# Performance work log

Hardware: AMD Instinct MI355X
Metric: run time of the kernel (lower is better)

The kernel has to match this reference:

```python
import jax, jax.numpy as jnp
import numpy as np

EPS = 1e-5
NPOINT = 1024
NSAMPLE = 32


def _bn(x, gamma, beta, axes):
    # batch-norm in training mode (biased variance), channel-last
    m = jnp.mean(x, axes, keepdims=True)
    v = jnp.var(x, axes, keepdims=True)
    return (x - m) * jax.lax.rsqrt(v + EPS) * gamma + beta


def _fps(xyz, npoint):
    # xyz: [B, N, 3] -> indices [B, npoint]; deterministic start at index 0
    xyz = jax.lax.stop_gradient(xyz)
    B, N, _ = xyz.shape

    def step(carry, _):
        dist, far = carry
        c = jnp.take_along_axis(xyz, far[:, None, None], axis=1)  # [B,1,3]
        d = jnp.sum((xyz - c) ** 2, -1)                            # [B,N]
        dist = jnp.minimum(dist, d)
        return (dist, jnp.argmax(dist, -1).astype(jnp.int32)), far

    init = (jnp.full((B, N), 1e10, xyz.dtype), jnp.zeros((B,), jnp.int32))
    _, idx = jax.lax.scan(step, init, None, length=npoint)
    return idx.T  # [B, npoint]


def _sqdist(src, dst):
    # [B,S,C],[B,N,C] -> [B,S,N]
    d = -2.0 * jnp.einsum('bsc,bnc->bsn', src, dst)
    d += jnp.sum(src ** 2, -1)[:, :, None]
    d += jnp.sum(dst ** 2, -1)[:, None, :]
    return d


def _gather(p, idx):
    # p: [B,N,C], idx: [B,...] -> [B,...,C]
    return jax.vmap(lambda a, i: a[i])(p, idx)


def setup_inputs() -> dict:
    key = jax.random.key(0)
    ks = jax.random.split(key, 12)
    B, N, D = 8, 4096, 64
    inp = {
        'xyz': jax.random.normal(ks[0], (B, 3, N), jnp.float32),
        'points': jax.random.normal(ks[1], (B, D, N), jnp.float32),
        # mlp convs (1x1 Conv2d == per-point linear): [out,in]
        'c1_w': jax.random.normal(ks[2], (64, 64), jnp.float32) / 8.0,
        'c1_b': jnp.zeros((64,), jnp.float32),
        'g1': jnp.ones((64,), jnp.float32), 'b1': jnp.zeros((64,), jnp.float32),
        'c2_w': jax.random.normal(ks[3], (128, 64), jnp.float32) / 8.0,
        'c2_b': jnp.zeros((128,), jnp.float32),
        'g2': jnp.ones((128,), jnp.float32), 'b2': jnp.zeros((128,), jnp.float32),
        # weightnet: 3 -> 8 -> 8 -> 16
        'w0_w': jax.random.normal(ks[4], (8, 3), jnp.float32) / np.sqrt(3.0),
        'w0_b': jnp.zeros((8,), jnp.float32),
        'w0_g': jnp.ones((8,), jnp.float32), 'w0_be': jnp.zeros((8,), jnp.float32),
        'w1_w': jax.random.normal(ks[5], (8, 8), jnp.float32) / np.sqrt(8.0),
        'w1_b': jnp.zeros((8,), jnp.float32),
        'w1_g': jnp.ones((8,), jnp.float32), 'w1_be': jnp.zeros((8,), jnp.float32),
        'w2_w': jax.random.normal(ks[6], (16, 8), jnp.float32) / np.sqrt(8.0),
        'w2_b': jnp.zeros((16,), jnp.float32),
        'w2_g': jnp.ones((16,), jnp.float32), 'w2_be': jnp.zeros((16,), jnp.float32),
        # final linear: 16*128 -> 128
        'lin_w': jax.random.normal(ks[7], (128, 16 * 128), jnp.float32) / np.sqrt(2048.0),
        'lin_b': jnp.zeros((128,), jnp.float32),
        'lg': jnp.ones((128,), jnp.float32), 'lb': jnp.zeros((128,), jnp.float32),
    }
    return inp


def reference(xyz, points, c1_w, c1_b, g1, b1, c2_w, c2_b, g2, b2,
              w0_w, w0_b, w0_g, w0_be, w1_w, w1_b, w1_g, w1_be,
              w2_w, w2_b, w2_g, w2_be, lin_w, lin_b, lg, lb):
    B = xyz.shape[0]
    X = jnp.transpose(xyz, (0, 2, 1))      # [B,N,3]
    P = jnp.transpose(points, (0, 2, 1))   # [B,N,D]

    fps_idx = _fps(X, NPOINT)                                      # [B,S]
    new_xyz = jnp.take_along_axis(X, fps_idx[:, :, None], axis=1)  # [B,S,3]

    sqr = _sqdist(jax.lax.stop_gradient(new_xyz), jax.lax.stop_gradient(X))
    _, nidx = jax.lax.top_k(-sqr, NSAMPLE)                         # [B,S,K]

    neigh_xyz = _gather(X, nidx)                                   # [B,S,K,3]
    off = neigh_xyz - new_xyz[:, :, None, :]                       # [B,S,K,3]
    f = _gather(P, nidx)                                           # [B,S,K,D]

    # per-point MLP (1x1 convs + BN2d over (B,K,S) + relu)
    for W, bias, g, be in ((c1_w, c1_b, g1, b1), (c2_w, c2_b, g2, b2)):
        f = jax.nn.relu(_bn(jnp.einsum('bskd,cd->bskc', f, W) + bias, g, be, (0, 1, 2)))

    # WeightNet on offsets
    w = off
    for W, bias, g, be in ((w0_w, w0_b, w0_g, w0_be),
                           (w1_w, w1_b, w1_g, w1_be),
                           (w2_w, w2_b, w2_g, w2_be)):
        w = jax.nn.relu(_bn(jnp.einsum('bskd,cd->bskc', w, W) + bias, g, be, (0, 1, 2)))

    # weighted aggregation over neighbors: [B,S,Cl,16] -> [B,S,Cl*16]
    feats = jnp.einsum('bskc,bskw->bscw', f, w).reshape(B, NPOINT, -1)
    y = feats @ lin_w.T + lin_b                                    # [B,S,128]
    y = jax.nn.relu(_bn(y, lg, lb, (0, 1)))

    return jnp.transpose(new_xyz, (0, 2, 1)), jnp.transpose(y, (0, 2, 1))
```

## Files before the change

kernel.cpp:

```cpp
#include <hip/hip_runtime.h>
#include <hip/hip_bf16.h>

#define BB 8
#define NN 4096
#define DD 64
#define SS 1024
#define KK 32
#define C1 64
#define C2 128

typedef unsigned int uint32;
typedef unsigned long long uint64;

constexpr int BSK = BB * SS * KK;
constexpr int BS  = BB * SS;

#define ST_S1_C1 0
#define ST_S2_C1 64
#define ST_S1_C2 128
#define ST_S2_C2 256
#define ST_S1_W0 384
#define ST_S2_W0 392
#define ST_S1_W1 400
#define ST_S2_W1 408
// ... 22 lines not shown
    uint64 u = (uint64)__double_as_longlong(x);
    int lo = (int)(uint32)u, hi = (int)(uint32)(u >> 32);
    int lo2 = __builtin_amdgcn_update_dpp(lo, lo, CTRL, 0xf, 0xf, false);
    int hi2 = __builtin_amdgcn_update_dpp(hi, hi, CTRL, 0xf, 0xf, false);
    return __longlong_as_double((long long)(((uint64)(uint32)hi2 << 32) | (uint32)lo2));
}
__device__ __forceinline__ double wave_max_pack(double k) {
    k = fmax(k, dpp_f64<0x111>(k));
    k = fmax(k, dpp_f64<0x112>(k));
    k = fmax(k, dpp_f64<0x114>(k));
    k = fmax(k, dpp_f64<0x118>(k));
    k = fmax(k, dpp_f64<0x142>(k));
    k = fmax(k, dpp_f64<0x143>(k));
    return k;
}
__device__ __forceinline__ double wave_min_pack(double k) {
    k = fmin(k, dpp_f64<0x111>(k));
    k = fmin(k, dpp_f64<0x112>(k));
    k = fmin(k, dpp_f64<0x114>(k));
    k = fmin(k, dpp_f64<0x118>(k));
    k = fmin(k, dpp_f64<0x142>(k));
    k = fmin(k, dpp_f64<0x143>(k));
    return k;
}
__device__ __forceinline__ uint64 bcast63_u64(double k) {
#if __has_builtin(__builtin_amdgcn_readlane)
    uint64 u = (uint64)__double_as_longlong(k);
    int lo = __builtin_amdgcn_readlane((int)(uint32)u, 63);
    int hi = __builtin_amdgcn_readlane((int)(uint32)(u >> 32), 63);
    return ((uint64)(uint32)hi << 32) | (uint32)lo;
#else
    return (uint64)__double_as_longlong(__shfl(k, 63));
#endif
}
#define FPS_WRITER_LANE 63
template <int CTRL>
__device__ __forceinline__ float dpp_mov_f32(float x) {
    int r = __builtin_amdgcn_update_dpp(__float_as_int(x), __float_as_int(x),
                                        CTRL, 0xf, 0xf, false);
    return __int_as_float(r);
}
__device__ __forceinline__ float wave_sum_f32(float v) {
    v += dpp_mov_f32<0x111>(v);
    v += dpp_mov_f32<0x112>(v);
    v += dpp_mov_f32<0x114>(v);
    v += dpp_mov_f32<0x118>(v);
    v += dpp_mov_f32<0x142>(v);
    v += dpp_mov_f32<0x143>(v);
    return v;
}
#define LIN_WRITER 63
#else
#define HAS_DPP 0
__device__ __forceinline__ double wave_max_pack(double k) {
#pragma unroll
    for (int m = 32; m >= 1; m >>= 1) k = fmax(k, __shfl_xor(k, m));
    return k;
}
__device__ __forceinline__ double wave_min_pack(double k) {
#pragma unroll
    for (int m = 32; m >= 1; m >>= 1) k = fmin(k, __shfl_xor(k, m));
    return k;
}
__device__ __forceinline__ uint64 bcast63_u64(double k) {
    return (uint64)__double_as_longlong(k);
}
#define FPS_WRITER_LANE 0
__device__ __forceinline__ float wave_sum_f32(float v) {
#pragma unroll
    for (int m = 32; m >= 1; m >>= 1) v += __shfl_xor(v, m);
    return v;
}
#define LIN_WRITER 0
#endif

__device__ __forceinline__ uint32 bf16rne(float x) {
    uint32 u = __float_as_uint(x);
    return (u + 0x7fffu + ((u >> 16) & 1u)) >> 16;
}

typedef __attribute__((ext_vector_type(8))) short bf16x8;
typedef __attribute__((ext_vector_type(4))) float f32x4v;

__global__ __launch_bounds__(256) void prep_fps_knn(const float* __restrict__ points,
                                                    __hip_bfloat16* __restrict__ ptsT,
                                                    const float* __restrict__ c1_w,
                                                    const float* __restrict__ c2_w,
                                                    const float* __restrict__ lin_w,
                                                    float* __restrict__ w1t,
                                                    float* __restrict__ w2t,
                                                    __hip_bfloat16* __restrict__ linB,
                                                    const float* __restrict__ xyz,
                                                    float* __restrict__ new_xyz,
                                                    float* __restrict__ out0,
                                                    int* __restrict__ progress,
                                                    int* __restrict__ nidx,
                                                    float* __restrict__ offs) {
    __shared__ __align__(16) char smu[82048];
    int t = threadIdx.x;
    int blk = blockIdx.x;
    if (blk < 8) {
        __builtin_amdgcn_s_setprio(3);
        float4* xyz4 = (float4*)smu;
        int* hist = (int*)(smu + 65536);
        double* slots = (double*)(smu + 69632);
        int b = blk;
        int wv = t >> 6, lane = t & 63;
        const float* base = xyz + (size_t)b * 3 * NN;
        float px[16], py[16], pz[16], dl[16];
        uint32 lidx[16];
#pragma unroll
        for (int i = 0; i < 16; i++) {
            int n = t + 256 * i;
            px[i] = base[n];
            py[i] = base[NN + n];
            pz[i] = base[2 * NN + n];
            float4 v; v.x = px[i]; v.y = py[i]; v.z = pz[i]; v.w = 0.f;
            xyz4[n] = v;
            dl[i] = 1e10f;
            lidx[i] = (uint32)(NN - 1 - n);
        }
        if (t == 0) hist[0] = 0;
        __syncthreads();
        int far = 0;
        for (int step = 1; step < SS; step++) {
            int p = step & 1;
            float4 c = xyz4[far];
            float cx = c.x, cy = c.y, cz = c.z;
            double k0 = 0.0, k1 = 0.0, k2 = 0.0, k3 = 0.0;
#pragma unroll
            for (int i = 0; i < 16; i++) {
                float dx = __fsub_rn(px[i], cx);
                float dy = __fsub_rn(py[i], cy);
                float dz = __fsub_rn(pz[i], cz);
                float d = __fadd_rn(__fadd_rn(__fmul_rn(dx, dx), __fmul_rn(dy, dy)),
                                    __fmul_rn(dz, dz));
                float nd = fminf(dl[i], d);
                dl[i] = nd;
                uint64 kbits = ((uint64)__float_as_uint(nd) << 32) | lidx[i];
                double kk = __longlong_as_double((long long)kbits);
                if ((i & 3) == 0) k0 = fmax(k0, kk);
                else if ((i & 3) == 1) k1 = fmax(k1, kk);
                else if ((i & 3) == 2) k2 = fmax(k2, kk);
                else k3 = fmax(k3, kk);
            }
            double kbest = fmax(fmax(k0, k1), fmax(k2, k3));
            kbest = wave_max_pack(kbest);
            if (lane == FPS_WRITER_LANE) slots[p * 4 + wv] = kbest;
            __syncthreads();
            double s0 = slots[p * 4 + 0], s1 = slots[p * 4 + 1];
            double s2 = slots[p * 4 + 2], s3 = slots[p * 4 + 3];
            double bk = fmax(fmax(s0, s1), fmax(s2, s3));
            uint64 kb = (uint64)__double_as_longlong(bk);
            int bbx = (NN - 1) - (int)(uint32)(kb & 0xffffffffull);
            far = bbx;
            if (t == 0) hist[step] = bbx;
            if ((step & 31) == 1 && step > 32) {
                if (t < 32) {
                    int s2p = step - 33 + t;
                    int idx2 = hist[s2p];
                    float4 v2 = xyz4[idx2];
                    size_t qq = (size_t)(b * SS + s2p) * 3;
                    new_xyz[qq + 0] = v2.x;
                    new_xyz[qq + 1] = v2.y;
                    new_xyz[qq + 2] = v2.z;
                }
                if (t == 0)
                    __hip_atomic_store(&progress[b], step - 1, __ATOMIC_RELEASE,
                                       __HIP_MEMORY_SCOPE_AGENT);
            }
        }
        __syncthreads();
        for (int s = t; s < SS; s += 256) {
            int idx = hist[s];
            float4 v = xyz4[idx];
            size_t q = (size_t)(b * SS + s);
            new_xyz[q * 3 + 0] = v.x;
            new_xyz[q * 3 + 1] = v.y;
            new_xyz[q * 3 + 2] = v.z;
            out0[(size_t)b * 3 * SS + 0 * SS + s] = v.x;
            out0[(size_t)b * 3 * SS + 1 * SS + s] = v.y;
            out0[(size_t)b * 3 * SS + 2 * SS + s] = v.z;
        }
        __threadfence();
        __syncthreads();
        if (t == 0)
            __hip_atomic_store(&progress[b], SS, __ATOMIC_RELEASE,
                               __HIP_MEMORY_SCOPE_AGENT);
        __builtin_amdgcn_s_setprio(0);
    } else if (blk < 520) {
        float (*tile)[65] = (float(*)[65])smu;
        int bb = blk - 8;
        int b = bb >> 6;
        int n0 = (bb & 63) * 64;
        for (int i = t; i < 4096; i += 256) {
            int d = i >> 6, n = i & 63;
            tile[d][n] = points[((size_t)b * DD + d) * NN + n0 + n];
        }
        __syncthreads();
        for (int i = t; i < 4096; i += 256) {
            int n = i >> 6, d = i & 63;
            ptsT[((size_t)b * NN + n0 + n) * DD + d] = __float2bfloat16(tile[d][n]);
        }
    } else if (blk < 1592) {
        int i = (blk - 520) * 256 + t;
        if (i < 4096) {
            int d = i >> 6, c = i & 63;
            w1t[d * 64 + c] = c1_w[c * 64 + d];
        }
        int j = i - 4096;
        if (j >= 0 && j < 8192) {
            int d = j >> 7, c = j & 127;
            w2t[d * 128 + c] = c2_w[c * 64 + d];
        }
        int l = i - 12288;
        if (l >= 0 && l < 262144) linB[l] = __float2bfloat16(lin_w[l]);
    } else {
        int cb = blk - 1592;
        int wv = t >> 6, lane = t & 63;
        int bq = cb & 7;
        int pos = ((cb >> 3) << 2) + wv;
        int q = bq * SS + pos;
        int needed = pos + 1;
        while (__hip_atomic_load(&progress[bq], __ATOMIC_ACQUIRE,
                                 __HIP_MEMORY_SCOPE_AGENT) < needed)
            __builtin_amdgcn_s_sleep(32);
        const float* base = xyz + (size_t)bq * 3 * NN;
        float sx = new_xyz[(size_t)q * 3 + 0];
        float sy = new_xyz[(size_t)q * 3 + 1];
        float sz = new_xyz[(size_t)q * 3 + 2];
        float s2 = __fadd_rn(__fadd_rn(__fmul_rn(sx, sx), __fmul_rn(sy, sy)), __fmul_rn(sz, sz));
        float dl[64];
#pragma unroll
        for (int i = 0; i < 64; i++) {
            int n = i * 64 + lane;
            float x = base[n], y = base[NN + n], z = base[2 * NN + n];
            float d2 = __fadd_rn(__fadd_rn(__fmul_rn(x, x), __fmul_rn(y, y)), __fmul_rn(z, z));
            float dot = __fadd_rn(__fadd_rn(__fmul_rn(sx, x), __fmul_rn(sy, y)), __fmul_rn(sz, z));
            float v = __fmul_rn(-2.0f, dot);
            v = __fadd_rn(v, s2);
            v = __fadd_rn(v, d2);
            dl[i] = v;
        }
        const float MASKF = __uint_as_float(0x7F7FFFFFu);
        unsigned long long excl = 0ull;
        for (int k = 0; k < KK; k++) {
            float best = MASKF;
            int bslot = 0;
#pragma unroll
            for (int i = 0; i < 64; i++) {
                bool ok = ((excl >> i) & 1ull) == 0ull;
                float v = ok ? dl[i] : MASKF;
                if (v < best) { best = v; bslot = i; }
            }
            uint64 kbits = ((uint64)__float_as_uint(best) << 32) |
                           (uint32)(bslot * 64 + lane);
            double kb = wave_min_pack(__longlong_as_double((long long)kbits));
            uint64 r = bcast63_u64(kb);
            int bi = (int)(uint32)(r & 0xffffffffull);
            if ((bi & 63) == lane) excl |= (1ull << (bi >> 6));
            if (lane == 0) {
                nidx[(size_t)q * KK + k] = bi;
                size_t oo = ((size_t)q * KK + k) * 3;
                offs[oo + 0] = __fsub_rn(base[bi], sx);
                offs[oo + 1] = __fsub_rn(base[NN + bi], sy);
                offs[oo + 2] = __fsub_rn(base[2 * NN + bi], sz);
            }
        }
    }
}

__device__ __forceinline__ void stage_pts(const __hip_bfloat16* __restrict__ ptsT,
                                          const int* __restrict__ nidx,
                                          int q, int b, int t, float* pts) {
    int k = t >> 3, d8 = t & 7;
    int nn = nidx[(size_t)q * KK + k];
    uint4 u = ((const uint4*)ptsT)[((size_t)b * NN + nn) * 8 + d8];
    float4 lo, hi;
    lo.x = __uint_as_float(u.x << 16); lo.y = __uint_as_float(u.x & 0xffff0000u);
    lo.z = __uint_as_float(u.y << 16); lo.w = __uint_as_float(u.y & 0xffff0000u);
    hi.x = __uint_as_float(u.z << 16); hi.y = __uint_as_float(u.z & 0xffff0000u);
    hi.z = __uint_as_float(u.w << 16); hi.w = __uint_as_float(u.w & 0xffff0000u);
    *(float4*)&pts[k * 64 + d8 * 8] = lo;
    *(float4*)&pts[k * 64 + d8 * 8 + 4] = hi;
}

__global__ __launch_bounds__(256) void pass_a(const __hip_bfloat16* __restrict__ ptsT,
                                              const int* __restrict__ nidx,
                                              const float* __restrict__ offs,
                                              const float* __restrict__ w1t,
                                              const float* __restrict__ c1_b,
                                              const float* __restrict__ w0_w,
                                              const float* __restrict__ w0_b,
                                              float* __restrict__ stats,
                                              float* __restrict__ f1pre,
                                              int emit_f1) {
    __shared__ __align__(16) float pts[2048];
    __shared__ float red1[256], red2[256];
    int blk = blockIdx.x, t = threadIdx.x;
    int b = blk >> 10;
    int slot = blk & (N_SLOTS - 1);
    stage_pts(ptsT, nidx, blk, b, t, pts);
    __syncthreads();
    int c = t & 63, kg = t >> 6;
    float bias = c1_b[c];
    float acc[8];
#pragma unroll
    for (int j = 0; j < 8; j++) acc[j] = bias;
    for (int d4 = 0; d4 < 16; d4++) {
        float w0 = w1t[(4 * d4 + 0) * 64 + c];
        float w1v = w1t[(4 * d4 + 1) * 64 + c];
        float w2v = w1t[(4 * d4 + 2) * 64 + c];
        float w3 = w1t[(4 * d4 + 3) * 64 + c];
#pragma unroll
        for (int j = 0; j < 8; j++) {
            const float4 p = *(const float4*)&pts[(kg + 4 * j) * 64 + 4 * d4];
            acc[j] = fmaf(p.x, w0, acc[j]);
            acc[j] = fmaf(p.y, w1v, acc[j]);
            acc[j] = fmaf(p.z, w2v, acc[j]);
            acc[j] = fmaf(p.w, w3, acc[j]);
        }
    }
    if (emit_f1) {
#pragma unroll
        for (int j = 0; j < 8; j++)
            f1pre[(size_t)blk * 2048 + j * 256 + t] = acc[j];
    }
    float s1 = 0.f, s2 = 0.f;
#pragma unroll
    for (int j = 0; j < 8; j++) { s1 += acc[j]; s2 += acc[j] * acc[j]; }
    red1[t] = s1;
    red2[t] = s2;
    __syncthreads();
    if (t < 64) {
        atomicAdd(&stats[slot * ST_STRIDE + ST_S1_C1 + t],
                  red1[t] + red1[t + 64] + red1[t + 128] + red1[t + 192]);
        atomicAdd(&stats[slot * ST_STRIDE + ST_S2_C1 + t],
                  red2[t] + red2[t + 64] + red2[t + 128] + red2[t + 192]);
    }
    int k0 = t >> 3, c0 = t & 7;
    size_t oo = ((size_t)blk * KK + k0) * 3;
    float h = w0_b[c0];
    h = fmaf(offs[oo + 0], w0_w[c0 * 3 + 0], h);
    h = fmaf(offs[oo + 1], w0_w[c0 * 3 + 1], h);
    h = fmaf(offs[oo + 2], w0_w[c0 * 3 + 2], h);
    __syncthreads();
    red1[t] = h;
    red2[t] = h * h;
    __syncthreads();
    if (t < 8) {
        float a = 0.f, q = 0.f;
        for (int j = t; j < 256; j += 8) { a += red1[j]; q += red2[j]; }
        atomicAdd(&stats[slot * ST_STRIDE + ST_S1_W0 + t], a);
        atomicAdd(&stats[slot * ST_STRIDE + ST_S2_W0 + t], q);
    }
}

__device__ __forceinline__ void fin_one(const float* stats, float* params,
                                        const float* g, const float* be,
                                        int s1o, int s2o, int ao, int co,
                                        int nch, float inv, int t) {
    if (t < nch) {
        float s1 = 0.f, s2 = 0.f;
        for (int s = 0; s < N_SLOTS; s++) {
            s1 += stats[s * ST_STRIDE + s1o + t];
            s2 += stats[s * ST_STRIDE + s2o + t];
        }
// ... 50 lines not shown
#pragma unroll
        for (int j = 0; j < 8; j++) acc[j] = bias;
        for (int d4 = 0; d4 < 16; d4++) {
            float w0 = w1t[(4 * d4 + 0) * 64 + c];
            float w1v = w1t[(4 * d4 + 1) * 64 + c];
            float w2v = w1t[(4 * d4 + 2) * 64 + c];
            float w3 = w1t[(4 * d4 + 3) * 64 + c];
#pragma unroll
            for (int j = 0; j < 8; j++) {
                const float4 p = *(const float4*)&pts[(kg + 4 * j) * 64 + 4 * d4];
                acc[j] = fmaf(p.x, w0, acc[j]);
                acc[j] = fmaf(p.y, w1v, acc[j]);
                acc[j] = fmaf(p.z, w2v, acc[j]);
                acc[j] = fmaf(p.w, w3, acc[j]);
            }
        }
#pragma unroll
        for (int j = 0; j < 8; j++)
            f1[(kg + 4 * j) * 64 + c] = fmaxf(fmaf(acc[j], a1, cc1), 0.f);
    }
    __syncthreads();
    {
        int c = t & 127, kg = t >> 7;
        float bias = c2_b[c];
        float acc[16];
#pragma unroll
        for (int j = 0; j < 16; j++) acc[j] = bias;
        for (int d4 = 0; d4 < 16; d4++) {
            float w0 = w2t[(4 * d4 + 0) * 128 + c];
            float w1v = w2t[(4 * d4 + 1) * 128 + c];
            float w2v = w2t[(4 * d4 + 2) * 128 + c];
            float w3 = w2t[(4 * d4 + 3) * 128 + c];
#pragma unroll
            for (int j = 0; j < 16; j++) {
                const float4 p = *(const float4*)&f1[(kg + 2 * j) * 64 + 4 * d4];
                acc[j] = fmaf(p.x, w0, acc[j]);
                acc[j] = fmaf(p.y, w1v, acc[j]);
                acc[j] = fmaf(p.z, w2v, acc[j]);
                acc[j] = fmaf(p.w, w3, acc[j]);
            }
        }
        float s1 = 0.f, s2 = 0.f;
#pragma unroll
        for (int j = 0; j < 16; j++) { s1 += acc[j]; s2 += acc[j] * acc[j]; }
        red1[t] = s1;
        red2[t] = s2;
    }
    __syncthreads();
    if (t < 128) {
        atomicAdd(&stats[slot * ST_STRIDE + ST_S1_C2 + t], red1[t] + red1[t + 128]);
        atomicAdd(&stats[slot * ST_STRIDE + ST_S2_C2 + t], red2[t] + red2[t + 128]);
    }
    {
        int k0 = t >> 3, c0 = t & 7;
        size_t oo = ((size_t)blk * KK + k0) * 3;
        float o0 = offs[oo], o1 = offs[oo + 1], o2 = offs[oo + 2];
        float h0[8];
#pragma unroll
        for (int j = 0; j < 8; j++) {
            float hh = w0_b[j];
            hh = fmaf(o0, w0_w[j * 3 + 0], hh);
            hh = fmaf(o1, w0_w[j * 3 + 1], hh);
            hh = fmaf(o2, w0_w[j * 3 + 2], hh);
            h0[j] = fmaxf(fmaf(hh, params[PA_A_W0 + j], params[PA_C_W0 + j]), 0.f);
        }
        float h = w1_b[c0];
#pragma unroll
        for (int j = 0; j < 8; j++) h = fmaf(h0[j], w1_w[c0 * 8 + j], h);
        __syncthreads();
        red1[t] = h;
        red2[t] = h * h;
        __syncthreads();
        if (t < 8) {
            float a = 0.f, q = 0.f;
            for (int j = t; j < 256; j += 8) { a += red1[j]; q += red2[j]; }
            atomicAdd(&stats[slot * ST_STRIDE + ST_S1_W1 + t], a);
            atomicAdd(&stats[slot * ST_STRIDE + ST_S2_W1 + t], q);
        }
    }
}

__global__ __launch_bounds__(256) void pass_b2(const float* __restrict__ f1pre,
                                               const float* __restrict__ offs,
                                               const float* __restrict__ w2t,
                                               const float* __restrict__ c2_b,
                                               const float* __restrict__ w0_w,
                                               const float* __restrict__ w0_b,
                                               const float* __restrict__ w1_w,
                                               const float* __restrict__ w1_b,
                                               const float* __restrict__ params,
                                               float* __restrict__ stats,
                                               float* __restrict__ f2pre) {
    __shared__ __align__(16) float f1[2048];
    __shared__ float red1[256], red2[256];
    int blk = blockIdx.x, t = threadIdx.x;
    int slot = blk & (N_SLOTS - 1);
    {
        int c = t & 63;
        float a1 = params[PA_A_C1 + c], cc1 = params[PA_C_C1 + c];
#pragma unroll
        for (int i = 0; i < 8; i++) {
            float v = f1pre[(size_t)blk * 2048 + i * 256 + t];
            f1[i * 256 + t] = fmaxf(fmaf(v, a1, cc1), 0.f);
        }
    }
    __syncthreads();
    {
        int c = t & 127, kg = t >> 7;
        float bias = c2_b[c];
        float acc[16];
#pragma unroll
        for (int j = 0; j < 16; j++) acc[j] = bias;
        for (int d4 = 0; d4 < 16; d4++) {
            float w0 = w2t[(4 * d4 + 0) * 128 + c];
            float w1v = w2t[(4 * d4 + 1) * 128 + c];
            float w2v = w2t[(4 * d4 + 2) * 128 + c];
            float w3 = w2t[(4 * d4 + 3) * 128 + c];
#pragma unroll
            for (int j = 0; j < 16; j++) {
                const float4 p = *(const float4*)&f1[(kg + 2 * j) * 64 + 4 * d4];
                acc[j] = fmaf(p.x, w0, acc[j]);
                acc[j] = fmaf(p.y, w1v, acc[j]);
                acc[j] = fmaf(p.z, w2v, acc[j]);
                acc[j] = fmaf(p.w, w3, acc[j]);
            }
        }
#pragma unroll
        for (int j = 0; j < 16; j++)
            f2pre[(size_t)blk * 4096 + j * 256 + t] = acc[j];
        float s1 = 0.f, s2 = 0.f;
#pragma unroll
        for (int j = 0; j < 16; j++) { s1 += acc[j]; s2 += acc[j] * acc[j]; }
        red1[t] = s1;
        red2[t] = s2;
    }
    __syncthreads();
    if (t < 128) {
        atomicAdd(&stats[slot * ST_STRIDE + ST_S1_C2 + t], red1[t] + red1[t + 128]);
        atomicAdd(&stats[slot * ST_STRIDE + ST_S2_C2 + t], red2[t] + red2[t + 128]);
    }
    {
        int k0 = t >> 3, c0 = t & 7;
        size_t oo = ((size_t)blk * KK + k0) * 3;
        float o0 = offs[oo], o1 = offs[oo + 1], o2 = offs[oo + 2];
        float h0[8];
#pragma unroll
        for (int j = 0; j < 8; j++) {
            float hh = w0_b[j];
            hh = fmaf(o0, w0_w[j * 3 + 0], hh);
            hh = fmaf(o1, w0_w[j * 3 + 1], hh);
            hh = fmaf(o2, w0_w[j * 3 + 2], hh);
            h0[j] = fmaxf(fmaf(hh, params[PA_A_W0 + j], params[PA_C_W0 + j]), 0.f);
        }
        float h = w1_b[c0];
#pragma unroll
        for (int j = 0; j < 8; j++) h = fmaf(h0[j], w1_w[c0 * 8 + j], h);
        __syncthreads();
        red1[t] = h;
        red2[t] = h * h;
        __syncthreads();
        if (t < 8) {
            float a = 0.f, q = 0.f;
            for (int j = t; j < 256; j += 8) { a += red1[j]; q += red2[j]; }
            atomicAdd(&stats[slot * ST_STRIDE + ST_S1_W1 + t], a);
            atomicAdd(&stats[slot * ST_STRIDE + ST_S2_W1 + t], q);
        }
    }
}

__global__ __launch_bounds__(256) void pass_w2(const float* __restrict__ offs,
                                               const float* __restrict__ w0_w,
                                               const float* __restrict__ w0_b,
                                               const float* __restrict__ w1_w,
                                               const float* __restrict__ w1_b,
                                               const float* __restrict__ w2_w,
                                               const float* __restrict__ w2_b,
                                               const float* __restrict__ params,
                                               float* __restrict__ stats) {
    int i = blockIdx.x * 256 + threadIdx.x;
    int slot = blockIdx.x & (N_SLOTS - 1);
    size_t oo = (size_t)i * 3;
    float o0 = offs[oo], o1 = offs[oo + 1], o2 = offs[oo + 2];
    float h0[8], h1[8];
#pragma unroll
    for (int j = 0; j < 8; j++) {
        float hh = w0_b[j];
        hh = fmaf(o0, w0_w[j * 3 + 0], hh);
        hh = fmaf(o1, w0_w[j * 3 + 1], hh);
        hh = fmaf(o2, w0_w[j * 3 + 2], hh);
        h0[j] = fmaxf(fmaf(hh, params[PA_A_W0 + j], params[PA_C_W0 + j]), 0.f);
    }
#pragma unroll
    for (int j = 0; j < 8; j++) {
        float hh = w1_b[j];
#pragma unroll
        for (int q = 0; q < 8; q++) hh = fmaf(h0[q], w1_w[j * 8 + q], hh);
        h1[j] = fmaxf(fmaf(hh, params[PA_A_W1 + j], params[PA_C_W1 + j]), 0.f);
    }
#pragma unroll
    for (int c = 0; c < 16; c++) {
        float h = w2_b[c];
#pragma unroll
        for (int q = 0; q < 8; q++) h = fmaf(h1[q], w2_w[c * 8 + q], h);
        float v = wave_sum_f32(h);
        float s = wave_sum_f32(h * h);
        if ((threadIdx.x & 63) == LIN_WRITER) {
            atomicAdd(&stats[slot * ST_STRIDE + ST_S1_W2 + c], v);
            atomicAdd(&stats[slot * ST_STRIDE + ST_S2_W2 + c], s);
        }
    }
}

__device__ __forceinline__ void weightnet_to_lds(const float* __restrict__ offs,
                                                 const float* __restrict__ w0_w,
                                                 const float* __restrict__ w0_b,
                                                 const float* __restrict__ w1_w,
                                                 const float* __restrict__ w1_b,
                                                 const float* __restrict__ w2_w,
                                                 const float* __restrict__ w2_b,
                                                 const float* __restrict__ params,
                                                 int blk, int t, float* wg) {
    for (int idx = t; idx < KK * 16; idx += 256) {
        int k = idx >> 4, cw = idx & 15;
        size_t oo = ((size_t)blk * KK + k) * 3;
        float o0 = offs[oo], o1 = offs[oo + 1], o2 = offs[oo + 2];
        float h0[8], h1[8];
#pragma unroll
        for (int j = 0; j < 8; j++) {
            float hh = w0_b[j];
            hh = fmaf(o0, w0_w[j * 3 + 0], hh);
            hh = fmaf(o1, w0_w[j * 3 + 1], hh);
            hh = fmaf(o2, w0_w[j * 3 + 2], hh);
            h0[j] = fmaxf(fmaf(hh, params[PA_A_W0 + j], params[PA_C_W0 + j]), 0.f);
        }
#pragma unroll
        for (int j = 0; j < 8; j++) {
            float hh = w1_b[j];
#pragma unroll
            for (int q = 0; q < 8; q++) hh = fmaf(h0[q], w1_w[j * 8 + q], hh);
            h1[j] = fmaxf(fmaf(hh, params[PA_A_W1 + j], params[PA_C_W1 + j]), 0.f);
// ... 267 lines not shown
        }
        const float inv = 1.f / (float)BS;
        float m = s1 * inv;
        float v = s2 * inv - m * m;
        float a = lg[t] * rsqrtf(v + 1e-5f);
        pa[t] = a;
        pc[t] = lb[t] - m * a;
    }
#pragma unroll
    for (int i = 0; i < 32; i++) {
        int idx = i * 256 + t;
        int s = idx >> 7, c = idx & 127;
        tile[s * 133 + c] = ypre[(((size_t)b << 10) + s0 + s) * 128 + c];
    }
    __syncthreads();
#pragma unroll
    for (int i = 0; i < 32; i++) {
        int idx = i * 256 + t;
        int c = idx >> 6, s = idx & 63;
        float v = tile[s * 133 + c];
        out1[((size_t)b * 128 + c) * 1024 + s0 + s] =
            fmaxf(fmaf(v, pa[c], pc[c]), 0.f);
    }
}

extern "C" void kernel_launch(void* const* d_in, const int* in_sizes, int n_in,
                              void* d_out, int out_size, void* d_ws, size_t ws_size,
                              hipStream_t stream) {
    const float* xyz    = (const float*)d_in[0];
    const float* points = (const float*)d_in[1];
    const float* c1_w = (const float*)d_in[2];
    const float* c1_b = (const float*)d_in[3];
    const float* g1   = (const float*)d_in[4];
    const float* b1   = (const float*)d_in[5];
    const float* c2_w = (const float*)d_in[6];
    const float* c2_b = (const float*)d_in[7];
    const float* g2   = (const float*)d_in[8];
    const float* b2   = (const float*)d_in[9];
    const float* w0_w = (const float*)d_in[10];
    const float* w0_b = (const float*)d_in[11];
    const float* w0_g = (const float*)d_in[12];
    const float* w0_be= (const float*)d_in[13];
    const float* w1_w = (const float*)d_in[14];
    const float* w1_b = (const float*)d_in[15];
    const float* w1_g = (const float*)d_in[16];
    const float* w1_be= (const float*)d_in[17];
    const float* w2_w = (const float*)d_in[18];
    const float* w2_b = (const float*)d_in[19];
    const float* w2_g = (const float*)d_in[20];
    const float* w2_be= (const float*)d_in[21];
    const float* lin_w= (const float*)d_in[22];
    const float* lin_b= (const float*)d_in[23];
    const float* lg   = (const float*)d_in[24];
    const float* lb   = (const float*)d_in[25];

    float* out0 = (float*)d_out;
    float* out1 = out0 + (size_t)BB * 3 * SS;

    char* wsb = (char*)d_ws;
    int*   nidx    = (int*)(wsb + 0);
    float* offs    = (float*)(wsb + 1048576);
    float* new_xyz = (float*)(wsb + 4194304);
    float* ypre    = (float*)(wsb + 4292608);
    __hip_bfloat16* ptsT = (__hip_bfloat16*)(wsb + 8486912);
    float* w1t     = (float*)(wsb + 12681216);
    float* w2t     = (float*)(wsb + 12697600);
    __hip_bfloat16* linB = (__hip_bfloat16*)(wsb + 12730368);
    float* stats   = (float*)(wsb + 13254656);
    float* params  = (float*)(wsb + 13434880);
    int*   progress= (int*)(wsb + 13436672);
    float* featsF  = (float*)(wsb + 13437696);
    float* f1pre   = featsF;
    float* f2pre   = (float*)(wsb + 80546560);

    const size_t NEED1 = 13437696ull + 67108864ull;
    const size_t NEED2 = 80546560ull + 134217728ull;
    const int tier = (ws_size >= NEED2) ? 2 : (ws_size >= NEED1) ? 1 : 0;

    hipMemsetAsync(stats, 0, N_SLOTS * ST_STRIDE * sizeof(float), stream);
    hipMemsetAsync(progress, 0, 64, stream);

    prep_fps_knn<<<3640, 256, 0, stream>>>(points, ptsT, c1_w, c2_w, lin_w, w1t, w2t,
                                           linB, xyz, new_xyz, out0,
                                           progress, nidx, offs);

    pass_a<<<BS, 256, 0, stream>>>(ptsT, nidx, offs, w1t, c1_b, w0_w, w0_b, stats,
                                   f1pre, tier == 2 ? 1 : 0);
    finalize_two<<<2, 128, 0, stream>>>(stats, params,
                                        g1, b1, ST_S1_C1, ST_S2_C1, PA_A_C1, PA_C_C1, 64, 1.f / BSK,
                                        w0_g, w0_be, ST_S1_W0, ST_S2_W0, PA_A_W0, PA_C_W0, 8, 1.f / BSK);

    if (tier == 2) {
        pass_b2<<<BS, 256, 0, stream>>>(f1pre, offs, w2t, c2_b,
                                        w0_w, w0_b, w1_w, w1_b, params, stats, f2pre);
    } else {
        pass_b<<<BS, 256, 0, stream>>>(ptsT, nidx, offs, w1t, c1_b, w2t, c2_b,
                                       w0_w, w0_b, w1_w, w1_b, params, stats);
    }
    finalize_two<<<2, 128, 0, stream>>>(stats, params,
                                        g2, b2, ST_S1_C2, ST_S2_C2, PA_A_C2, PA_C_C2, 128, 1.f / BSK,
                                        w1_g, w1_be, ST_S1_W1, ST_S2_W1, PA_A_W1, PA_C_W1, 8, 1.f / BSK);

    pass_w2<<<BSK / 256, 256, 0, stream>>>(offs, w0_w, w0_b, w1_w, w1_b, w2_w, w2_b,
                                           params, stats);
    finalize_bn<<<1, 128, 0, stream>>>(stats, params, w2_g, w2_be,
                                       ST_S1_W2, ST_S2_W2, PA_A_W2, PA_C_W2, 16, 1.f / BSK);

    if (tier == 2) {
        tail_nl2<<<BS, 256, 0, stream>>>(f2pre, offs, w0_w, w0_b, w1_w, w1_b,
                                         w2_w, w2_b, params, featsF);
        linear_mm16<<<BS / 16, 256, 0, stream>>>(featsF, linB, lin_b, stats, ypre);
    } else {
        fused_tail_nl<<<BS, 256, 0, stream>>>(ptsT, nidx, offs, w1t, c1_b, w2t, c2_b,
                                              w0_w, w0_b, w1_w, w1_b, w2_w, w2_b,
                                              params, featsF);
        linear_mm16<<<BS / 16, 256, 0, stream>>>(featsF, linB, lin_b, stats, ypre);
    }

    bn_y<<<BB * 16, 256, 0, stream>>>(ypre, stats, lg, lb, out1);
}
```

Before: 1.054 ms.

## Fuse pass_a conv1 and weightnet-layer0 stats into the FPS/kNN kernel

Result: slower. 1.087 ms (+3.2%).

```diff
diff --git a/kernel.cpp b/kernel.cpp
--- a/kernel.cpp
+++ b/kernel.cpp
@@ -128,6 +128,21 @@
 typedef __attribute__((ext_vector_type(8))) short bf16x8;
 typedef __attribute__((ext_vector_type(4))) float f32x4v;
 
+__device__ __forceinline__ void stage_pts(const __hip_bfloat16* __restrict__ ptsT,
+                                          const int* __restrict__ nidx,
+                                          int q, int b, int t, float* pts) {
+    int k = t >> 3, d8 = t & 7;
+    int nn = nidx[(size_t)q * KK + k];
+    uint4 u = ((const uint4*)ptsT)[((size_t)b * NN + nn) * 8 + d8];
+    float4 lo, hi;
+    lo.x = __uint_as_float(u.x << 16); lo.y = __uint_as_float(u.x & 0xffff0000u);
+    lo.z = __uint_as_float(u.y << 16); lo.w = __uint_as_float(u.y & 0xffff0000u);
+    hi.x = __uint_as_float(u.z << 16); hi.y = __uint_as_float(u.z & 0xffff0000u);
+    hi.z = __uint_as_float(u.w << 16); hi.w = __uint_as_float(u.w & 0xffff0000u);
+    *(float4*)&pts[k * 64 + d8 * 8] = lo;
+    *(float4*)&pts[k * 64 + d8 * 8 + 4] = hi;
+}
+
 __global__ __launch_bounds__(256) void prep_fps_knn(const float* __restrict__ points,
                                                     __hip_bfloat16* __restrict__ ptsT,
                                                     const float* __restrict__ c1_w,
@@ -141,7 +156,13 @@
                                                     float* __restrict__ out0,
                                                     int* __restrict__ progress,
                                                     int* __restrict__ nidx,
-                                                    float* __restrict__ offs) {
+                                                    float* __restrict__ offs,
+                                                    const float* __restrict__ c1_b,
+                                                    const float* __restrict__ w0_w,
+                                                    const float* __restrict__ w0_b,
+                                                    float* __restrict__ stats,
+                                                    float* __restrict__ f1pre,
+                                                    int fuse_a) {
     __shared__ __align__(16) char smu[82048];
     int t = threadIdx.x;
     int blk = blockIdx.x;
@@ -248,6 +269,11 @@
             int n = i >> 6, d = i & 63;
             ptsT[((size_t)b * NN + n0 + n) * DD + d] = __float2bfloat16(tile[d][n]);
         }
+        __threadfence();
+        __syncthreads();
+        if (t == 0)
+            __hip_atomic_fetch_add(&progress[8], 1, __ATOMIC_RELEASE,
+                                   __HIP_MEMORY_SCOPE_AGENT);
     } else if (blk < 1592) {
         int i = (blk - 520) * 256 + t;
         if (i < 4096) {
@@ -261,74 +287,134 @@
         }
         int l = i - 12288;
         if (l >= 0 && l < 262144) linB[l] = __float2bfloat16(lin_w[l]);
+        __threadfence();
+        __syncthreads();
+        if (t == 0)
+            __hip_atomic_fetch_add(&progress[8], 1, __ATOMIC_RELEASE,
+                                   __HIP_MEMORY_SCOPE_AGENT);
     } else {
         int cb = blk - 1592;
         int wv = t >> 6, lane = t & 63;
         int bq = cb & 7;
-        int pos = ((cb >> 3) << 2) + wv;
+        int p0 = (cb >> 3) << 2;
+        int pos = p0 + wv;
         int q = bq * SS + pos;
         int needed = pos + 1;
         while (__hip_atomic_load(&progress[bq], __ATOMIC_ACQUIRE,
                                  __HIP_MEMORY_SCOPE_AGENT) < needed)
             __builtin_amdgcn_s_sleep(32);
         const float* base = xyz + (size_t)bq * 3 * NN;
-        float sx = new_xyz[(size_t)q * 3 + 0];
-        float sy = new_xyz[(size_t)q * 3 + 1];
-        float sz = new_xyz[(size_t)q * 3 + 2];
-        float s2 = __fadd_rn(__fadd_rn(__fmul_rn(sx, sx), __fmul_rn(sy, sy)), __fmul_rn(sz, sz));
-        float dl[64];
-#pragma unroll
-        for (int i = 0; i < 64; i++) {
-            int n = i * 64 + lane;
-            float x = base[n], y = base[NN + n], z = base[2 * NN + n];
-            float d2 = __fadd_rn(__fadd_rn(__fmul_rn(x, x), __fmul_rn(y, y)), __fmul_rn(z, z));
-            float dot = __fadd_rn(__fadd_rn(__fmul_rn(sx, x), __fmul_rn(sy, y)), __fmul_rn(sz, z));
-            float v = __fmul_rn(-2.0f, dot);
-            v = __fadd_rn(v, s2);
-            v = __fadd_rn(v, d2);
-            dl[i] = v;
-        }
-        const float MASKF = __uint_as_float(0x7F7FFFFFu);
-        unsigned long long excl = 0ull;
-        for (int k = 0; k < KK; k++) {
-            float best = MASKF;
-            int bslot = 0;
+        {
+            float sx = new_xyz[(size_t)q * 3 + 0];
+            float sy = new_xyz[(size_t)q * 3 + 1];
+            float sz = new_xyz[(size_t)q * 3 + 2];
+            float s2 = __fadd_rn(__fadd_rn(__fmul_rn(sx, sx), __fmul_rn(sy, sy)),
+                                 __fmul_rn(sz, sz));
+            float dl[64];
 #pragma unroll
             for (int i = 0; i < 64; i++) {
-                bool ok = ((excl >> i) & 1ull) == 0ull;
-                float v = ok ? dl[i] : MASKF;
-                if (v < best) { best = v; bslot = i; }
+                int n = i * 64 + lane;
+                float x = base[n], y = base[NN + n], z = base[2 * NN + n];
+                float d2 = __fadd_rn(__fadd_rn(__fmul_rn(x, x), __fmul_rn(y, y)), __fmul_rn(z, z));
+                float dot = __fadd_rn(__fadd_rn(__fmul_rn(sx, x), __fmul_rn(sy, y)), __fmul_rn(sz, z));
+                float v = __fmul_rn(-2.0f, dot);
+                v = __fadd_rn(v, s2);
+                v = __fadd_rn(v, d2);
+                dl[i] = v;
             }
-            uint64 kbits = ((uint64)__float_as_uint(best) << 32) |
-                           (uint32)(bslot * 64 + lane);
-            double kb = wave_min_pack(__longlong_as_double((long long)kbits));
-            uint64 r = bcast63_u64(kb);
-            int bi = (int)(uint32)(r & 0xffffffffull);
-            if ((bi & 63) == lane) excl |= (1ull << (bi >> 6));
-            if (lane == 0) {
-                nidx[(size_t)q * KK + k] = bi;
-                size_t oo = ((size_t)q * KK + k) * 3;
-                offs[oo + 0] = __fsub_rn(base[bi], sx);
-                offs[oo + 1] = __fsub_rn(base[NN + bi], sy);
-                offs[oo + 2] = __fsub_rn(base[2 * NN + bi], sz);
+            const float MASKF = __uint_as_float(0x7F7FFFFFu);
+            unsigned long long excl = 0ull;
+            for (int k = 0; k < KK; k++) {
+                float best = MASKF;
+                int bslot = 0;
+#pragma unroll
+                for (int i = 0; i < 64; i++) {
+                    bool ok = ((excl >> i) & 1ull) == 0ull;
+                    float v = ok ? dl[i] : MASKF;
+                    if (v < best) { best = v; bslot = i; }
+                }
+                uint64 kbits = ((uint64)__float_as_uint(best) << 32) |
+                               (uint32)(bslot * 64 + lane);
+                double kb = wave_min_pack(__longlong_as_double((long long)kbits));
+                uint64 r = bcast63_u64(kb);
+                int bi = (int)(uint32)(r & 0xffffffffull);
+                if ((bi & 63) == lane) excl |= (1ull << (bi >> 6));
+                if (lane == 0) {
+                    nidx[(size_t)q * KK + k] = bi;
+                    size_t oo = ((size_t)q * KK + k) * 3;
+                    offs[oo + 0] = __fsub_rn(base[bi], sx);
+                    offs[oo + 1] = __fsub_rn(base[NN + bi], sy);
+                    offs[oo + 2] = __fsub_rn(base[2 * NN + bi], sz);
+                }
             }
         }
-    }
-}
-
-__device__ __forceinline__ void stage_pts(const __hip_bfloat16* __restrict__ ptsT,
-                                          const int* __restrict__ nidx,
-                                          int q, int b, int t, float* pts) {
-    int k = t >> 3, d8 = t & 7;
-    int nn = nidx[(size_t)q * KK + k];
-    uint4 u = ((const uint4*)ptsT)[((size_t)b * NN + nn) * 8 + d8];
-    float4 lo, hi;
-    lo.x = __uint_as_float(u.x << 16); lo.y = __uint_as_float(u.x & 0xffff0000u);
-    lo.z = __uint_as_float(u.y << 16); lo.w = __uint_as_float(u.y & 0xffff0000u);
-    hi.x = __uint_as_float(u.z << 16); hi.y = __uint_as_float(u.z & 0xffff0000u);
-    hi.z = __uint_as_float(u.w << 16); hi.w = __uint_as_float(u.w & 0xffff0000u);
-    *(float4*)&pts[k * 64 + d8 * 8] = lo;
-    *(float4*)&pts[k * 64 + d8 * 8 + 4] = hi;
+        if (!fuse_a) return;
+        if (t == 0) {
+            while (__hip_atomic_load(&progress[8], __ATOMIC_ACQUIRE,
+                                     __HIP_MEMORY_SCOPE_AGENT) < 1584)
+                __builtin_amdgcn_s_sleep(16);
+        }
+        __syncthreads();
+        float* cpts = (float*)smu;
+        float* red1 = (float*)(smu + 8192);
+        float* red2 = (float*)(smu + 9216);
+        for (int j4 = 0; j4 < 4; j4++) {
+            int qq = bq * SS + p0 + j4;
+            int slotq = qq & (N_SLOTS - 1);
+            stage_pts(ptsT, nidx, qq, bq, t, cpts);
+            __syncthreads();
+            int c = t & 63, kg = t >> 6;
+            float bias = c1_b[c];
+            float acc[8];
+#pragma unroll
+            for (int j = 0; j < 8; j++) acc[j] = bias;
+            for (int d4 = 0; d4 < 16; d4++) {
+                float w0 = w1t[(4 * d4 + 0) * 64 + c];
+                float w1v = w1t[(4 * d4 + 1) * 64 + c];
+                float w2v = w1t[(4 * d4 + 2) * 64 + c];
+                float w3 = w1t[(4 * d4 + 3) * 64 + c];
+#pragma unroll
+                for (int j = 0; j < 8; j++) {
+                    const float4 p = *(const float4*)&cpts[(kg + 4 * j) * 64 + 4 * d4];
+                    acc[j] = fmaf(p.x, w0, acc[j]);
+                    acc[j] = fmaf(p.y, w1v, acc[j]);
+                    acc[j] = fmaf(p.z, w2v, acc[j]);
+                    acc[j] = fmaf(p.w, w3, acc[j]);
+                }
+            }
+#pragma unroll
+            for (int j = 0; j < 8; j++)
+                f1pre[(size_t)qq * 2048 + j * 256 + t] = acc[j];
+            float s1 = 0.f, s2 = 0.f;
+#pragma unroll
+            for (int j = 0; j < 8; j++) { s1 += acc[j]; s2 += acc[j] * acc[j]; }
+            red1[t] = s1;
+            red2[t] = s2;
+            __syncthreads();
+            if (t < 64) {
+                atomicAdd(&stats[slotq * ST_STRIDE + ST_S1_C1 + t],
+                          red1[t] + red1[t + 64] + red1[t + 128] + red1[t + 192]);
+                atomicAdd(&stats[slotq * ST_STRIDE + ST_S2_C1 + t],
+                          red2[t] + red2[t + 64] + red2[t + 128] + red2[t + 192]);
+            }
+            int k0 = t >> 3, c0 = t & 7;
+            size_t oo = ((size_t)qq * KK + k0) * 3;
+            float h = w0_b[c0];
+            h = fmaf(offs[oo + 0], w0_w[c0 * 3 + 0], h);
+            h = fmaf(offs[oo + 1], w0_w[c0 * 3 + 1], h);
+            h = fmaf(offs[oo + 2], w0_w[c0 * 3 + 2], h);
+            __syncthreads();
+            red1[t] = h;
+            red2[t] = h * h;
+            __syncthreads();
+            if (t < 8) {
+                float a = 0.f, qv = 0.f;
+                for (int j = t; j < 256; j += 8) { a += red1[j]; qv += red2[j]; }
+                atomicAdd(&stats[slotq * ST_STRIDE + ST_S1_W0 + t], a);
+                atomicAdd(&stats[slotq * ST_STRIDE + ST_S2_W0 + t], qv);
+            }
+        }
+    }
 }
 
 __global__ __launch_bounds__(256) void pass_a(const __hip_bfloat16* __restrict__ ptsT,
@@ -1052,10 +1138,14 @@
 
     prep_fps_knn<<<3640, 256, 0, stream>>>(points, ptsT, c1_w, c2_w, lin_w, w1t, w2t,
                                            linB, xyz, new_xyz, out0,
-                                           progress, nidx, offs);
-
-    pass_a<<<BS, 256, 0, stream>>>(ptsT, nidx, offs, w1t, c1_b, w0_w, w0_b, stats,
-                                   f1pre, tier == 2 ? 1 : 0);
+                                           progress, nidx, offs,
+                                           c1_b, w0_w, w0_b, stats, f1pre,
+                                           tier == 2 ? 1 : 0);
+
+    if (tier != 2) {
+        pass_a<<<BS, 256, 0, stream>>>(ptsT, nidx, offs, w1t, c1_b, w0_w, w0_b, stats,
+                                       f1pre, 0);
+    }
     finalize_two<<<2, 128, 0, stream>>>(stats, params,
                                         g1, b1, ST_S1_C1, ST_S2_C1, PA_A_C1, PA_C_C1, 64, 1.f / BSK,
                                         w0_g, w0_be, ST_S1_W0, ST_S2_W0, PA_A_W0, PA_C_W0, 8, 1.f / BSK);
```

## Use split-bf16 MFMA for conv2 matmul in pass_b2

Applied to the files above, without the earlier changes.

Result: faster. 990.7 us (-6.0%).

```diff
diff --git a/kernel.cpp b/kernel.cpp
--- a/kernel.cpp
+++ b/kernel.cpp
@@ -128,6 +128,21 @@
 typedef __attribute__((ext_vector_type(8))) short bf16x8;
 typedef __attribute__((ext_vector_type(4))) float f32x4v;
 
+__device__ __forceinline__ void stage_pts(const __hip_bfloat16* __restrict__ ptsT,
+                                          const int* __restrict__ nidx,
+                                          int q, int b, int t, float* pts) {
+    int k = t >> 3, d8 = t & 7;
+    int nn = nidx[(size_t)q * KK + k];
+    uint4 u = ((const uint4*)ptsT)[((size_t)b * NN + nn) * 8 + d8];
+    float4 lo, hi;
+    lo.x = __uint_as_float(u.x << 16); lo.y = __uint_as_float(u.x & 0xffff0000u);
+    lo.z = __uint_as_float(u.y << 16); lo.w = __uint_as_float(u.y & 0xffff0000u);
+    hi.x = __uint_as_float(u.z << 16); hi.y = __uint_as_float(u.z & 0xffff0000u);
+    hi.z = __uint_as_float(u.w << 16); hi.w = __uint_as_float(u.w & 0xffff0000u);
+    *(float4*)&pts[k * 64 + d8 * 8] = lo;
+    *(float4*)&pts[k * 64 + d8 * 8 + 4] = hi;
+}
+
 __global__ __launch_bounds__(256) void prep_fps_knn(const float* __restrict__ points,
                                                     __hip_bfloat16* __restrict__ ptsT,
                                                     const float* __restrict__ c1_w,
@@ -141,7 +156,8 @@
                                                     float* __restrict__ out0,
                                                     int* __restrict__ progress,
                                                     int* __restrict__ nidx,
-                                                    float* __restrict__ offs) {
+                                                    float* __restrict__ offs,
+                                                    int pack_w2) {
     __shared__ __align__(16) char smu[82048];
     int t = threadIdx.x;
     int blk = blockIdx.x;
@@ -256,8 +272,22 @@
         }
         int j = i - 4096;
         if (j >= 0 && j < 8192) {
-            int d = j >> 7, c = j & 127;
-            w2t[d * 128 + c] = c2_w[c * 64 + d];
+            if (!pack_w2) {
+                int d = j >> 7, c = j & 127;
+                w2t[d * 128 + c] = c2_w[c * 64 + d];
+            } else {
+                int jj = j & 7, lnn = (j >> 3) & 15, lgg = (j >> 7) & 3;
+                int nf = (j >> 9) & 7, s = (j >> 12) & 1;
+                int d = s * 32 + lgg * 8 + jj;
+                int c = nf * 16 + lnn;
+                float v = c2_w[c * 64 + d];
+                uint32 hb = bf16rne(v);
+                float hif = __uint_as_float(hb << 16);
+                uint32 lb2 = bf16rne(v - hif);
+                unsigned short* w2p = (unsigned short*)w2t;
+                w2p[j] = (unsigned short)hb;
+                w2p[8192 + j] = (unsigned short)lb2;
+            }
         }
         int l = i - 12288;
         if (l >= 0 && l < 262144) linB[l] = __float2bfloat16(lin_w[l]);
@@ -314,21 +344,6 @@
             }
         }
     }
-}
-
-__device__ __forceinline__ void stage_pts(const __hip_bfloat16* __restrict__ ptsT,
-                                          const int* __restrict__ nidx,
-                                          int q, int b, int t, float* pts) {
-    int k = t >> 3, d8 = t & 7;
-    int nn = nidx[(size_t)q * KK + k];
-    uint4 u = ((const uint4*)ptsT)[((size_t)b * NN + nn) * 8 + d8];
-    float4 lo, hi;
-    lo.x = __uint_as_float(u.x << 16); lo.y = __uint_as_float(u.x & 0xffff0000u);
-    lo.z = __uint_as_float(u.y << 16); lo.w = __uint_as_float(u.y & 0xffff0000u);
-    hi.x = __uint_as_float(u.z << 16); hi.y = __uint_as_float(u.z & 0xffff0000u);
-    hi.z = __uint_as_float(u.w << 16); hi.w = __uint_as_float(u.w & 0xffff0000u);
-    *(float4*)&pts[k * 64 + d8 * 8] = lo;
-    *(float4*)&pts[k * 64 + d8 * 8 + 4] = hi;
 }
 
 __global__ __launch_bounds__(256) void pass_a(const __hip_bfloat16* __restrict__ ptsT,
@@ -545,7 +560,7 @@
 
 __global__ __launch_bounds__(256) void pass_b2(const float* __restrict__ f1pre,
                                                const float* __restrict__ offs,
-                                               const float* __restrict__ w2t,
+                                               const unsigned short* __restrict__ w2pack,
                                                const float* __restrict__ c2_b,
                                                const float* __restrict__ w0_w,
                                                const float* __restrict__ w0_b,
@@ -554,7 +569,8 @@
                                                const float* __restrict__ params,
                                                float* __restrict__ stats,
                                                float* __restrict__ f2pre) {
-    __shared__ __align__(16) float f1[2048];
+    __shared__ __align__(16) unsigned short f1h[32 * 72];
+    __shared__ __align__(16) unsigned short f1l[32 * 72];
     __shared__ float red1[256], red2[256];
     int blk = blockIdx.x, t = threadIdx.x;
     int slot = blk & (N_SLOTS - 1);
@@ -563,44 +579,79 @@
         float a1 = params[PA_A_C1 + c], cc1 = params[PA_C_C1 + c];
 #pragma unroll
         for (int i = 0; i < 8; i++) {
-            float v = f1pre[(size_t)blk * 2048 + i * 256 + t];
-            f1[i * 256 + t] = fmaxf(fmaf(v, a1, cc1), 0.f);
-        }
-    }
-    __syncthreads();
+            int e = i * 256 + t;
+            float v = f1pre[(size_t)blk * 2048 + e];
+            float f = fmaxf(fmaf(v, a1, cc1), 0.f);
+            int k = e >> 6, d = e & 63;
+            uint32 hb = bf16rne(f);
+            f1h[k * 72 + d] = (unsigned short)hb;
+            f1l[k * 72 + d] = (unsigned short)bf16rne(f - __uint_as_float(hb << 16));
+        }
+    }
+    __syncthreads();
+    int lane = t & 63, w = t >> 6;
+    int lg = lane >> 4, ln = lane & 15;
+    f32x4v acc00 = {0.f, 0.f, 0.f, 0.f};
+    f32x4v acc01 = {0.f, 0.f, 0.f, 0.f};
+    f32x4v acc10 = {0.f, 0.f, 0.f, 0.f};
+    f32x4v acc11 = {0.f, 0.f, 0.f, 0.f};
+#pragma unroll
+    for (int s = 0; s < 2; s++) {
+        int ao = s * 32 + lg * 8;
+        bf16x8 ah0 = *(const bf16x8*)&f1h[(ln) * 72 + ao];
+        bf16x8 ah1 = *(const bf16x8*)&f1h[(16 + ln) * 72 + ao];
+        bf16x8 al0 = *(const bf16x8*)&f1l[(ln) * 72 + ao];
+        bf16x8 al1 = *(const bf16x8*)&f1l[(16 + ln) * 72 + ao];
+        int nf0 = w * 2, nf1 = w * 2 + 1;
+        int b0off = (((s * 8 + nf0) * 4 + lg) * 16 + ln) * 8;
+        int b1off = (((s * 8 + nf1) * 4 + lg) * 16 + ln) * 8;
+        bf16x8 bh0 = *(const bf16x8*)&w2pack[b0off];
+        bf16x8 bl0 = *(const bf16x8*)&w2pack[8192 + b0off];
+        bf16x8 bh1 = *(const bf16x8*)&w2pack[b1off];
+        bf16x8 bl1 = *(const bf16x8*)&w2pack[8192 + b1off];
+        acc00 = __builtin_amdgcn_mfma_f32_16x16x32_bf16(ah0, bh0, acc00, 0, 0, 0);
+        acc00 = __builtin_amdgcn_mfma_f32_16x16x32_bf16(al0, bh0, acc00, 0, 0, 0);
+        acc00 = __builtin_amdgcn_mfma_f32_16x16x32_bf16(ah0, bl0, acc00, 0, 0, 0);
+        acc01 = __builtin_amdgcn_mfma_f32_16x16x32_bf16(ah0, bh1, acc01, 0, 0, 0);
+        acc01 = __builtin_amdgcn_mfma_f32_16x16x32_bf16(al0, bh1, acc01, 0, 0, 0);
+        acc01 = __builtin_amdgcn_mfma_f32_16x16x32_bf16(ah0, bl1, acc01, 0, 0, 0);
+        acc10 = __builtin_amdgcn_mfma_f32_16x16x32_bf16(ah1, bh0, acc10, 0, 0, 0);
+        acc10 = __builtin_amdgcn_mfma_f32_16x16x32_bf16(al1, bh0, acc10, 0, 0, 0);
+        acc10 = __builtin_amdgcn_mfma_f32_16x16x32_bf16(ah1, bl0, acc10, 0, 0, 0);
+        acc11 = __builtin_amdgcn_mfma_f32_16x16x32_bf16(ah1, bh1, acc11, 0, 0, 0);
+        acc11 = __builtin_amdgcn_mfma_f32_16x16x32_bf16(al1, bh1, acc11, 0, 0, 0);
+        acc11 = __builtin_amdgcn_mfma_f32_16x16x32_bf16(ah1, bl1, acc11, 0, 0, 0);
+    }
     {
-        int c = t & 127, kg = t >> 7;
-        float bias = c2_b[c];
-        float acc[16];
-#pragma unroll
-        for (int j = 0; j < 16; j++) acc[j] = bias;
-        for (int d4 = 0; d4 < 16; d4++) {
-            float w0 = w2t[(4 * d4 + 0) * 128 + c];
-            float w1v = w2t[(4 * d4 + 1) * 128 + c];
-            float w2v = w2t[(4 * d4 + 2) * 128 + c];
-            float w3 = w2t[(4 * d4 + 3) * 128 + c];
-#pragma unroll
-            for (int j = 0; j < 16; j++) {
-                const float4 p = *(const float4*)&f1[(kg + 2 * j) * 64 + 4 * d4];
-                acc[j] = fmaf(p.x, w0, acc[j]);
-                acc[j] = fmaf(p.y, w1v, acc[j]);
-                acc[j] = fmaf(p.z, w2v, acc[j]);
-                acc[j] = fmaf(p.w, w3, acc[j]);
-            }
-        }
-#pragma unroll
-        for (int j = 0; j < 16; j++)
-            f2pre[(size_t)blk * 4096 + j * 256 + t] = acc[j];
-        float s1 = 0.f, s2 = 0.f;
-#pragma unroll
-        for (int j = 0; j < 16; j++) { s1 += acc[j]; s2 += acc[j] * acc[j]; }
-        red1[t] = s1;
-        red2[t] = s2;
-    }
-    __syncthreads();
-    if (t < 128) {
-        atomicAdd(&stats[slot * ST_STRIDE + ST_S1_C2 + t], red1[t] + red1[t + 128]);
-        atomicAdd(&stats[slot * ST_STRIDE + ST_S2_C2 + t], red2[t] + red2[t + 128]);
+        int c0 = w * 32 + ln;
+        int c1c = w * 32 + 16 + ln;
+        float b0 = c2_b[c0], b1 = c2_b[c1c];
+        float p10 = 0.f, p20 = 0.f, p11 = 0.f, p21 = 0.f;
+#pragma unroll
+        for (int r = 0; r < 4; r++) {
+            int k0 = lg * 4 + r;
+            int k1 = 16 + lg * 4 + r;
+            float v00 = acc00[r] + b0;
+            float v01 = acc01[r] + b1;
+            float v10 = acc10[r] + b0;
+            float v11 = acc11[r] + b1;
+            f2pre[(size_t)blk * 4096 + k0 * 128 + c0]  = v00;
+            f2pre[(size_t)blk * 4096 + k0 * 128 + c1c] = v01;
+            f2pre[(size_t)blk * 4096 + k1 * 128 + c0]  = v10;
+            f2pre[(size_t)blk * 4096 + k1 * 128 + c1c] = v11;
+            p10 += v00 + v10; p20 += v00 * v00 + v10 * v10;
+            p11 += v01 + v11; p21 += v01 * v01 + v11 * v11;
+        }
+        p10 += __shfl_xor(p10, 16); p10 += __shfl_xor(p10, 32);
+        p20 += __shfl_xor(p20, 16); p20 += __shfl_xor(p20, 32);
+        p11 += __shfl_xor(p11, 16); p11 += __shfl_xor(p11, 32);
+        p21 += __shfl_xor(p21, 16); p21 += __shfl_xor(p21, 32);
+        if (lg == 0) {
+            atomicAdd(&stats[slot * ST_STRIDE + ST_S1_C2 + c0], p10);
+            atomicAdd(&stats[slot * ST_STRIDE + ST_S2_C2 + c0], p20);
+            atomicAdd(&stats[slot * ST_STRIDE + ST_S1_C2 + c1c], p11);
+            atomicAdd(&stats[slot * ST_STRIDE + ST_S2_C2 + c1c], p21);
+        }
     }
     {
         int k0 = t >> 3, c0 = t & 7;
@@ -618,7 +669,6 @@
         float h = w1_b[c0];
 #pragma unroll
         for (int j = 0; j < 8; j++) h = fmaf(h0[j], w1_w[c0 * 8 + j], h);
-        __syncthreads();
         red1[t] = h;
         red2[t] = h * h;
         __syncthreads();
@@ -1052,7 +1102,8 @@
 
     prep_fps_knn<<<3640, 256, 0, stream>>>(points, ptsT, c1_w, c2_w, lin_w, w1t, w2t,
                                            linB, xyz, new_xyz, out0,
-                                           progress, nidx, offs);
+                                           progress, nidx, offs,
+                                           tier == 2 ? 1 : 0);
 
     pass_a<<<BS, 256, 0, stream>>>(ptsT, nidx, offs, w1t, c1_b, w0_w, w0_b, stats,
                                    f1pre, tier == 2 ? 1 : 0);
@@ -1061,7 +1112,7 @@
                                         w0_g, w0_be, ST_S1_W0, ST_S2_W0, PA_A_W0, PA_C_W0, 8, 1.f / BSK);
 
     if (tier == 2) {
-        pass_b2<<<BS, 256, 0, stream>>>(f1pre, offs, w2t, c2_b,
+        pass_b2<<<BS, 256, 0, stream>>>(f1pre, offs, (const unsigned short*)w2t, c2_b,
                                         w0_w, w0_b, w1_w, w1_b, params, stats, f2pre);
     } else {
         pass_b<<<BS, 256, 0, stream>>>(ptsT, nidx, offs, w1t, c1_b, w2t, c2_b,
```
